# Optimization experiments

Hardware: AMD Instinct MI355X
Metric: run time of the kernel (lower is better)

The kernel has to match this reference:

```python
import itertools
import jax, jax.numpy as jnp
import numpy as np

# ---- constant tables / bases ----
Y_TABLE_NP = np.array([
    [16, 11, 10, 16, 24, 40, 51, 61],
    [12, 12, 14, 19, 26, 58, 60, 55],
    [14, 13, 16, 24, 40, 57, 69, 56],
    [14, 17, 22, 29, 51, 87, 80, 62],
    [18, 22, 37, 56, 68, 109, 103, 77],
    [24, 35, 55, 64, 81, 104, 113, 92],
    [49, 64, 78, 87, 103, 121, 120, 101],
    [72, 92, 95, 98, 112, 100, 103, 99]], dtype=np.float32)
C_TABLE_NP = np.full((8, 8), 99, dtype=np.float32)
C_TABLE_NP[:4, :4] = np.array([[17, 18, 24, 47], [18, 21, 26, 66],
                               [24, 26, 56, 99], [47, 66, 99, 99]], dtype=np.float32)

def _bases():
    dct = np.zeros((8, 8, 8, 8), dtype=np.float32)
    idct = np.zeros((8, 8, 8, 8), dtype=np.float32)
    for x, y, u, v in itertools.product(range(8), repeat=4):
        dct[x, y, u, v] = np.cos((2 * x + 1) * u * np.pi / 16) * np.cos((2 * y + 1) * v * np.pi / 16)
        idct[x, y, u, v] = np.cos((2 * u + 1) * x * np.pi / 16) * np.cos((2 * v + 1) * y * np.pi / 16)
    alpha = np.array([1.0 / np.sqrt(2)] + [1.0] * 7, dtype=np.float32)
    ao = np.outer(alpha, alpha).astype(np.float32)
    return jnp.asarray(dct), jnp.asarray(ao * 0.25), jnp.asarray(idct), jnp.asarray(ao)

DCT_T, DCT_SCALE, IDCT_T, ALPHA = _bases()
FACTOR = 0.4  # quality_to_factor(80) = (200 - 2*80)/100


def diff_round(x):
    r = jnp.round(x)
    return r + (x - r) ** 3


def _blocks(img):  # (B,H,W) -> (B, H*W/64, 8, 8)
    B, H, W = img.shape
    return img.reshape(B, H // 8, 8, W // 8, 8).transpose(0, 1, 3, 2, 4).reshape(B, -1, 8, 8)


def _merge(patches, H, W):  # (B, N, 8, 8) -> (B, H, W)
    B = patches.shape[0]
    return patches.reshape(B, H // 8, W // 8, 8, 8).transpose(0, 1, 3, 2, 4).reshape(B, H, W)


def setup_inputs() -> dict:
    key = jax.random.key(0)
    image = jax.random.uniform(key, (32, 3, 512, 512), dtype=jnp.float32)
    return {"image": image,
            "y_table": jnp.asarray(Y_TABLE_NP),
            "c_table": jnp.asarray(C_TABLE_NP)}


def reference(image, y_table, c_table):
    B, _, H, W = image.shape
    x = image * 255.0
    # RGB -> YCbCr (matrix stored transposed in torch, tensordot over channel)
    rgb2ycc = jnp.array([[0.299, 0.587, 0.114],
                         [-0.168736, -0.331264, 0.5],
                         [0.5, -0.418688, -0.081312]], dtype=jnp.float32)
    shift = jnp.array([0.0, 128.0, 128.0], dtype=jnp.float32)
    ycc = jnp.einsum('bchw,kc->bhwk', x, rgb2ycc) + shift  # (B,H,W,3)
    y = ycc[..., 0]
    # chroma subsampling: 2x2 average pool
    def pool2(ch):
        return ch.reshape(B, H // 2, 2, W // 2, 2).mean(axis=(2, 4))
    cb = pool2(ycc[..., 1])
    cr = pool2(ycc[..., 2])

    def compress(ch, table):
        blk = _blocks(ch) - 128.0
        d = DCT_SCALE * jnp.einsum('bnxy,xyuv->bnuv', blk, DCT_T)
        return diff_round(d / (table * FACTOR))

    yq = compress(y, y_table)
    cbq = compress(cb, c_table)
    crq = compress(cr, c_table)

    def decompress(q, table, h, w):
        d = (q * (table * FACTOR)) * ALPHA
        blk = 0.25 * jnp.einsum('bnuv,uvxy->bnxy', d, IDCT_T) + 128.0
        return _merge(blk, h, w)

    y_rec = decompress(yq, y_table, H, W)
    cb_rec = decompress(cbq, c_table, H // 2, W // 2)
    cr_rec = decompress(crq, c_table, H // 2, W // 2)

    def up2(ch):
        b, h, w = ch.shape
        return jnp.broadcast_to(ch[:, :, None, :, None], (b, h, 2, w, 2)).reshape(b, 2 * h, 2 * w)

    ycc_rec = jnp.stack([y_rec, up2(cb_rec), up2(cr_rec)], axis=-1)  # (B,H,W,3)
    ycc2rgb = jnp.array([[1.0, 0.0, 1.402],
                         [1.0, -0.344136, -0.714136],
                         [1.0, 1.772, 0.0]], dtype=jnp.float32)
    shift2 = jnp.array([0.0, -128.0, -128.0], dtype=jnp.float32)
    rgb = jnp.einsum('bhwk,ck->bhwc', ycc_rec + shift2, ycc2rgb)
    rgb = rgb.transpose(0, 3, 1, 2)  # (B,3,H,W)
    return jnp.clip(rgb, 0.0, 255.0) / 255.0
```

## Files before the change

kernel.cpp:

```cpp
#include <hip/hip_runtime.h>
#include <math.h>

#define IMG_H 512
#define IMG_W 512
#define IMG_HW (IMG_H * IMG_W)

namespace {

constexpr float CFv[9] = {
    1.0f,
    0.98078528040323044913f,
    0.92387953251128675613f,
    0.83146961230254523708f,
    0.70710678118654752440f,
    0.55557023301960222474f,
    0.38268343236508977173f,
    0.19509032201612826785f,
    0.0f
};

struct CTab {
    float  cf[8][8];
    double cd[8][8];
    float  aof[8][8];
    float  scalef[8][8];
};

constexpr CTab make_ctab() {
    CTab t{};
    for (int y = 0; y < 8; y++) {
        for (int v = 0; v < 8; v++) {
            int a = ((2 * y + 1) * v) & 31;
            if (a > 16) a = 32 - a;
            float val = (a <= 8) ? CFv[a] : -CFv[16 - a];
            t.cf[y][v] = val;
            t.cd[y][v] = (double)val;
        }
    }
    constexpr float A0 = 0.70710678118654752440f;
    for (int u = 0; u < 8; u++) {
        for (int v = 0; v < 8; v++) {
            float au = (u == 0) ? A0 : 1.0f;
            float av = (v == 0) ? A0 : 1.0f;
            float ao = au * av;
            t.aof[u][v] = ao;
            t.scalef[u][v] = ao * 0.25f;
        }
    }
    return t;
}

constexpr CTab CT = make_ctab();

constexpr double YC0 = (double)0.299f    * 255.0;
constexpr double YC1 = (double)0.587f    * 255.0;
constexpr double YC2 = (double)0.114f    * 255.0;
constexpr double CB0 = (double)-0.168736f * 255.0;
constexpr double CB1 = (double)-0.331264f * 255.0;
constexpr double CB2 = (double)0.5f      * 255.0;
constexpr double CR0 = (double)0.5f      * 255.0;
constexpr double CR1 = (double)-0.418688f * 255.0;
constexpr double CR2 = (double)-0.081312f * 255.0;

#define OFF_CBP 8448
#define OFF_CRP 10624
#define OFF_QY  12800
#define OFF_QC  13952
#define SMEM_BYTES 15104

__device__ __forceinline__ void xpose8_d(double v[8]) {
    const int l = threadIdx.x & 7;
    #pragma unroll
    for (int m = 1; m < 8; m <<= 1) {
        #pragma unroll
        for (int k = 0; k < 8; k++) {
            if ((k & m) == 0) {
                const int kp = k | m;
                double send = (l & m) ? v[k] : v[kp];
                double recv = __shfl_xor(send, m);
                v[k]  = (l & m) ? recv : v[k];
                v[kp] = (l & m) ? v[kp] : recv;
            }
        }
    }
}

__device__ __forceinline__ void xpose8_f(float v[8]) {
    const int l = threadIdx.x & 7;
    #pragma unroll
    for (int m = 1; m < 8; m <<= 1) {
        #pragma unroll
        for (int k = 0; k < 8; k++) {
            if ((k & m) == 0) {
                const int kp = k | m;
                float send = (l & m) ? v[k] : v[kp];
                float recv = __shfl_xor(send, m);
                v[k]  = (l & m) ? recv : v[k];
                v[kp] = (l & m) ? v[kp] : recv;
            }
        }
    }
}

}

__global__ void __launch_bounds__(256, 6) djpeg_kernel(
    const float* __restrict__ img,
    const float* __restrict__ ytab,
    const float* __restrict__ ctab,
    float* __restrict__ out)
{
    __shared__ __align__(16) unsigned char smem[SMEM_BYTES];
    double* lY  = (double*)(smem);
    double* cbP = (double*)(smem + OFF_CBP);
    double* crP = (double*)(smem + OFF_CRP);
    double* qY  = (double*)(smem + OFF_QY);
    double* qC  = (double*)(smem + OFF_QC);
    float* yR  = (float*)(smem);
    float* cbR = (float*)(smem + 4224);
    float* crR = (float*)(smem + 5312);

    const int t  = threadIdx.x;
    const int X0 = blockIdx.x * 64;
    const int Y0 = blockIdx.y * 16;
    const int bi = blockIdx.z;

    if (t < 128) {
        const float* tab = (t < 64) ? ytab : ctab;
        double* q = (t < 64) ? qY : qC;
        int e = t & 63, u = e >> 3, v = e & 7;
        float tfacf = tab[e] * 0.4f;
        double tf = (double)tfacf;
        q[v * 18 + 2 * u]     = (double)CT.scalef[u][v] / tf;
        q[v * 18 + 2 * u + 1] = tf * (double)CT.aof[u][v];
    }

    {
        const int x = t & 63, yb = t >> 6;
        double accb[2] = {0.0, 0.0}, accr[2] = {0.0, 0.0};
        size_t base = ((size_t)bi * 3) * IMG_HW + (size_t)Y0 * IMG_W + X0 + x;
        #pragma unroll
        for (int i = 0; i < 4; i++) {
            int y = yb * 4 + i;
            size_t p = base + (size_t)y * IMG_W;
            double R = (double)img[p];
            double G = (double)img[p + IMG_HW];
            double B = (double)img[p + 2 * IMG_HW];
            double Yv = YC0 * R + YC1 * G + YC2 * B - 128.0;
            double Cb = CB0 * R + CB1 * G + CB2 * B;
            double Cr = CR0 * R + CR1 * G + CR2 * B;
            lY[y * 66 + x] = Yv;
            accb[i >> 1] += Cb;
            accr[i >> 1] += Cr;
        }
        #pragma unroll
        for (int p2 = 0; p2 < 2; p2++) {
            double hb = accb[p2] + __shfl_xor(accb[p2], 1);
            double hr = accr[p2] + __shfl_xor(accr[p2], 1);
            if ((x & 1) == 0) {
                int pr = yb * 2 + p2;
                cbP[pr * 34 + (x >> 1)] = hb * 0.25;
                crP[pr * 34 + (x >> 1)] = hr * 0.25;
            }
        }
    }
    __syncthreads();

    const bool act = (t < 192);
    const int r = t & 7;
    const double* src = lY;
    const double* qtab = qY;
    float* dstR = yR;
    if (act) {
        if (t < 128) {
            int g = t >> 3, by = g >> 3, bx = g & 7;
            src  = lY + (by * 8 + r) * 66 + bx * 8;
            dstR = yR + (by * 8 + r) * 66 + bx * 8;
            qtab = qY;
        } else {
            int c = t - 128;
            int isCr = c >> 5;
            int g2 = (c >> 3) & 3;
            src  = (isCr ? crP : cbP) + r * 34 + g2 * 8;
            dstR = (isCr ? crR : cbR) + r * 34 + g2 * 8;
            qtab = qC;
        }
    }
    const float addv = (t < 128) ? 128.0f : 0.0f;

    double s1[8];
    if (act) {
        double a[8];
        #pragma unroll
        for (int y = 0; y < 8; y++) a[y] = src[y];
        double e[4], o[4];
        #pragma unroll
        for (int i = 0; i < 4; i++) { e[i] = a[i] + a[7 - i]; o[i] = a[i] - a[7 - i]; }
        #pragma unroll
        for (int v = 0; v < 8; v += 2) {
            s1[v]     = e[0] * CT.cd[0][v]     + e[1] * CT.cd[1][v]     + e[2] * CT.cd[2][v]     + e[3] * CT.cd[3][v];
            s1[v + 1] = o[0] * CT.cd[0][v + 1] + o[1] * CT.cd[1][v + 1] + o[2] * CT.cd[2][v + 1] + o[3] * CT.cd[3][v + 1];
        }
        xpose8_d(s1);
    }

    float mrow[8];
    if (act) {
        double e[4], o[4];
        #pragma unroll
        for (int i = 0; i < 4; i++) { e[i] = s1[i] + s1[7 - i]; o[i] = s1[i] - s1[7 - i]; }
        double D[8];
        #pragma unroll
        for (int u = 0; u < 8; u += 2) {
            D[u]     = e[0] * CT.cd[0][u]     + e[1] * CT.cd[1][u]     + e[2] * CT.cd[2][u]     + e[3] * CT.cd[3][u];
            D[u + 1] = o[0] * CT.cd[0][u + 1] + o[1] * CT.cd[1][u + 1] + o[2] * CT.cd[2][u + 1] + o[3] * CT.cd[3][u + 1];
        }
        float dq[8];
        #pragma unroll
        for (int u = 0; u < 8; u++) {
            double fs = qtab[r * 18 + 2 * u];
            double ds = qtab[r * 18 + 2 * u + 1];
            double xq = D[u] * fs;
            double rq = rint(xq);
            double ee = xq - rq;
            dq[u] = (float)((rq + ee * ee * ee) * ds);
        }
        #pragma unroll
        for (int x = 0; x < 4; x++) {
            float E = dq[0] * CT.cf[x][0] + dq[2] * CT.cf[x][2] + dq[4] * CT.cf[x][4] + dq[6] * CT.cf[x][6];
            float O = dq[1] * CT.cf[x][1] + dq[3] * CT.cf[x][3] + dq[5] * CT.cf[x][5] + dq[7] * CT.cf[x][7];
            mrow[x]     = E + O;
            mrow[7 - x] = E - O;
        }
        xpose8_f(mrow);
    }

    __syncthreads();

    if (act) {
        #pragma unroll
        for (int y = 0; y < 4; y++) {
            float E = mrow[0] * CT.cf[y][0] + mrow[2] * CT.cf[y][2] + mrow[4] * CT.cf[y][4] + mrow[6] * CT.cf[y][6];
            float O = mrow[1] * CT.cf[y][1] + mrow[3] * CT.cf[y][3] + mrow[5] * CT.cf[y][5] + mrow[7] * CT.cf[y][7];
            dstR[y]     = 0.25f * (E + O) + addv;
            dstR[7 - y] = 0.25f * (E - O) + addv;
        }
    }
    __syncthreads();

    {
        const int x = t & 63, yb = t >> 6;
        size_t base = ((size_t)bi * 3) * IMG_HW + (size_t)Y0 * IMG_W + X0 + x;
        #pragma unroll
        for (int i = 0; i < 4; i++) {
            int y = yb * 4 + i;
            float Yv = yR[y * 66 + x];
            float Cb = cbR[(y >> 1) * 34 + (x >> 1)];
            float Cr = crR[(y >> 1) * 34 + (x >> 1)];
            float Rr = fmaf(1.402f, Cr, Yv);
            float Gg = Yv - 0.344136f * Cb - 0.714136f * Cr;
            float Bb = fmaf(1.772f, Cb, Yv);
            Rr = fminf(fmaxf(Rr, 0.0f), 255.0f) * (1.0f / 255.0f);
            Gg = fminf(fmaxf(Gg, 0.0f), 255.0f) * (1.0f / 255.0f);
            Bb = fminf(fmaxf(Bb, 0.0f), 255.0f) * (1.0f / 255.0f);
            size_t p = base + (size_t)y * IMG_W;
            out[p] = Rr;
            out[p + IMG_HW] = Gg;
            out[p + 2 * IMG_HW] = Bb;
        }
    }
}

extern "C" void kernel_launch(void* const* d_in, const int* in_sizes, int n_in,
                              void* d_out, int out_size, void* d_ws, size_t ws_size,
                              hipStream_t stream) {
    (void)n_in; (void)out_size; (void)d_ws; (void)ws_size;
    const float* img = (const float*)d_in[0];
    const float* yt  = (const float*)d_in[1];
    const float* ct  = (const float*)d_in[2];
    float* out = (float*)d_out;
    int B = in_sizes[0] / (3 * IMG_HW);
    dim3 grid(IMG_W / 64, IMG_H / 16, B);
    djpeg_kernel<<<grid, dim3(256, 1, 1), 0, stream>>>(img, yt, ct, out);
}
```

Before: 185.1 us.

## Widen tile to 128 columns, process two DCT blocks per thread, vectorize I/O

Each block now covers a 16x128 tile instead of 16x64, halving the grid. Every active thread transforms two 8x8 blocks (luma plus a second luma or chroma block), so all 192 active threads do twice the work. Global loads and stores use float4, and the chroma 2x2 averaging now uses a shuffle across half-waves. Shared memory nearly doubles and launch bounds drop to 4 blocks per SM, which reduces occupancy while raising per-thread ILP and memory transaction width.

```diff
diff --git a/kernel.cpp b/kernel.cpp
--- a/kernel.cpp
+++ b/kernel.cpp
@@ -52,21 +52,23 @@
 
 constexpr CTab CT = make_ctab();
 
-constexpr double YC0 = (double)0.299f    * 255.0;
-constexpr double YC1 = (double)0.587f    * 255.0;
-constexpr double YC2 = (double)0.114f    * 255.0;
+constexpr double YC0 = (double)0.299f     * 255.0;
+constexpr double YC1 = (double)0.587f     * 255.0;
+constexpr double YC2 = (double)0.114f     * 255.0;
 constexpr double CB0 = (double)-0.168736f * 255.0;
 constexpr double CB1 = (double)-0.331264f * 255.0;
-constexpr double CB2 = (double)0.5f      * 255.0;
-constexpr double CR0 = (double)0.5f      * 255.0;
+constexpr double CB2 = (double)0.5f       * 255.0;
+constexpr double CR0 = (double)0.5f       * 255.0;
 constexpr double CR1 = (double)-0.418688f * 255.0;
 constexpr double CR2 = (double)-0.081312f * 255.0;
 
-#define OFF_CBP 8448
-#define OFF_CRP 10624
-#define OFF_QY  12800
-#define OFF_QC  13952
-#define SMEM_BYTES 15104
+#define OFF_CBP 16640
+#define OFF_CRP 20864
+#define OFF_QY  25088
+#define OFF_QC  26240
+#define SMEM_BYTES 27392
+#define OFF_CBR 8448
+#define OFF_CRR 10560
 
 __device__ __forceinline__ void xpose8_d(double v[8]) {
     const int l = threadIdx.x & 7;
@@ -102,9 +104,58 @@
     }
 }
 
-}
-
-__global__ void __launch_bounds__(256, 6) djpeg_kernel(
+__device__ __forceinline__ void fdct8_d(const double a[8], double s[8]) {
+    double e[4], o[4];
+    #pragma unroll
+    for (int i = 0; i < 4; i++) { e[i] = a[i] + a[7 - i]; o[i] = a[i] - a[7 - i]; }
+    #pragma unroll
+    for (int v = 0; v < 8; v += 2) {
+        s[v]     = e[0] * CT.cd[0][v]     + e[1] * CT.cd[1][v]     + e[2] * CT.cd[2][v]     + e[3] * CT.cd[3][v];
+        s[v + 1] = o[0] * CT.cd[0][v + 1] + o[1] * CT.cd[1][v + 1] + o[2] * CT.cd[2][v + 1] + o[3] * CT.cd[3][v + 1];
+    }
+}
+
+__device__ __forceinline__ void quant_idct_u(const double s1[8], const double* qtab, int r, float m[8]) {
+    double e[4], o[4];
+    #pragma unroll
+    for (int i = 0; i < 4; i++) { e[i] = s1[i] + s1[7 - i]; o[i] = s1[i] - s1[7 - i]; }
+    double D[8];
+    #pragma unroll
+    for (int u = 0; u < 8; u += 2) {
+        D[u]     = e[0] * CT.cd[0][u]     + e[1] * CT.cd[1][u]     + e[2] * CT.cd[2][u]     + e[3] * CT.cd[3][u];
+        D[u + 1] = o[0] * CT.cd[0][u + 1] + o[1] * CT.cd[1][u + 1] + o[2] * CT.cd[2][u + 1] + o[3] * CT.cd[3][u + 1];
+    }
+    float dq[8];
+    #pragma unroll
+    for (int u = 0; u < 8; u++) {
+        double2 q = *(const double2*)&qtab[r * 18 + 2 * u];
+        double xq = D[u] * q.x;
+        double rq = rint(xq);
+        double ee = xq - rq;
+        dq[u] = (float)((rq + ee * ee * ee) * q.y);
+    }
+    #pragma unroll
+    for (int x = 0; x < 4; x++) {
+        float E = dq[0] * CT.cf[x][0] + dq[2] * CT.cf[x][2] + dq[4] * CT.cf[x][4] + dq[6] * CT.cf[x][6];
+        float O = dq[1] * CT.cf[x][1] + dq[3] * CT.cf[x][3] + dq[5] * CT.cf[x][5] + dq[7] * CT.cf[x][7];
+        m[x]     = E + O;
+        m[7 - x] = E - O;
+    }
+}
+
+__device__ __forceinline__ void idct_v_store(const float m[8], float* dst, float addv) {
+    #pragma unroll
+    for (int y = 0; y < 4; y++) {
+        float E = m[0] * CT.cf[y][0] + m[2] * CT.cf[y][2] + m[4] * CT.cf[y][4] + m[6] * CT.cf[y][6];
+        float O = m[1] * CT.cf[y][1] + m[3] * CT.cf[y][3] + m[5] * CT.cf[y][5] + m[7] * CT.cf[y][7];
+        dst[y]     = 0.25f * (E + O) + addv;
+        dst[7 - y] = 0.25f * (E - O) + addv;
+    }
+}
+
+}
+
+__global__ void __launch_bounds__(256, 4) djpeg_kernel(
     const float* __restrict__ img,
     const float* __restrict__ ytab,
     const float* __restrict__ ctab,
@@ -117,11 +168,11 @@
     double* qY  = (double*)(smem + OFF_QY);
     double* qC  = (double*)(smem + OFF_QC);
     float* yR  = (float*)(smem);
-    float* cbR = (float*)(smem + 4224);
-    float* crR = (float*)(smem + 5312);
+    float* cbR = (float*)(smem + OFF_CBR);
+    float* crR = (float*)(smem + OFF_CRR);
 
     const int t  = threadIdx.x;
-    const int X0 = blockIdx.x * 64;
+    const int X0 = blockIdx.x * 128;
     const int Y0 = blockIdx.y * 16;
     const int bi = blockIdx.z;
 
@@ -136,31 +187,39 @@
     }
 
     {
-        const int x = t & 63, yb = t >> 6;
-        double accb[2] = {0.0, 0.0}, accr[2] = {0.0, 0.0};
-        size_t base = ((size_t)bi * 3) * IMG_HW + (size_t)Y0 * IMG_W + X0 + x;
-        #pragma unroll
-        for (int i = 0; i < 4; i++) {
-            int y = yb * 4 + i;
+        const int xg = t & 31, row0 = t >> 5;
+        size_t base = ((size_t)bi * 3) * IMG_HW + (size_t)Y0 * IMG_W + X0 + 4 * xg;
+        #pragma unroll
+        for (int i = 0; i < 2; i++) {
+            int y = row0 + 8 * i;
             size_t p = base + (size_t)y * IMG_W;
-            double R = (double)img[p];
-            double G = (double)img[p + IMG_HW];
-            double B = (double)img[p + 2 * IMG_HW];
-            double Yv = YC0 * R + YC1 * G + YC2 * B - 128.0;
-            double Cb = CB0 * R + CB1 * G + CB2 * B;
-            double Cr = CR0 * R + CR1 * G + CR2 * B;
-            lY[y * 66 + x] = Yv;
-            accb[i >> 1] += Cb;
-            accr[i >> 1] += Cr;
-        }
-        #pragma unroll
-        for (int p2 = 0; p2 < 2; p2++) {
-            double hb = accb[p2] + __shfl_xor(accb[p2], 1);
-            double hr = accr[p2] + __shfl_xor(accr[p2], 1);
-            if ((x & 1) == 0) {
-                int pr = yb * 2 + p2;
-                cbP[pr * 34 + (x >> 1)] = hb * 0.25;
-                crP[pr * 34 + (x >> 1)] = hr * 0.25;
+            const float4 Rv = *(const float4*)(img + p);
+            const float4 Gv = *(const float4*)(img + p + IMG_HW);
+            const float4 Bv = *(const float4*)(img + p + 2 * IMG_HW);
+            const float rr[4] = {Rv.x, Rv.y, Rv.z, Rv.w};
+            const float gg[4] = {Gv.x, Gv.y, Gv.z, Gv.w};
+            const float bb[4] = {Bv.x, Bv.y, Bv.z, Bv.w};
+            double Yd[4], Cbv[4], Crv[4];
+            #pragma unroll
+            for (int k = 0; k < 4; k++) {
+                double R = (double)rr[k], G = (double)gg[k], B = (double)bb[k];
+                Yd[k]  = YC0 * R + YC1 * G + YC2 * B - 128.0;
+                Cbv[k] = CB0 * R + CB1 * G + CB2 * B;
+                Crv[k] = CR0 * R + CR1 * G + CR2 * B;
+            }
+            double2* w = (double2*)&lY[y * 130 + 4 * xg];
+            w[0] = make_double2(Yd[0], Yd[1]);
+            w[1] = make_double2(Yd[2], Yd[3]);
+            double cb01 = Cbv[0] + Cbv[1], cb23 = Cbv[2] + Cbv[3];
+            double cr01 = Crv[0] + Crv[1], cr23 = Crv[2] + Crv[3];
+            cb01 += __shfl_xor(cb01, 32);
+            cb23 += __shfl_xor(cb23, 32);
+            cr01 += __shfl_xor(cr01, 32);
+            cr23 += __shfl_xor(cr23, 32);
+            if ((t & 32) == 0) {
+                int yh = y >> 1;
+                *(double2*)&cbP[yh * 66 + 2 * xg] = make_double2(cb01 * 0.25, cb23 * 0.25);
+                *(double2*)&crP[yh * 66 + 2 * xg] = make_double2(cr01 * 0.25, cr23 * 0.25);
             }
         }
     }
@@ -168,105 +227,89 @@
 
     const bool act = (t < 192);
     const int r = t & 7;
-    const double* src = lY;
-    const double* qtab = qY;
-    float* dstR = yR;
+    const int g0 = t >> 3;
+    const double* src0 = lY;  const double* src1 = lY;
+    const double* qt1 = qY;
+    float* dst0 = yR;  float* dst1 = yR;
+    float addv1 = 128.0f;
     if (act) {
-        if (t < 128) {
-            int g = t >> 3, by = g >> 3, bx = g & 7;
-            src  = lY + (by * 8 + r) * 66 + bx * 8;
-            dstR = yR + (by * 8 + r) * 66 + bx * 8;
-            qtab = qY;
+        {
+            int by = (g0 >> 4), bx = g0 & 15;
+            src0 = lY + (by * 8 + r) * 130 + bx * 8;
+            dst0 = yR + (by * 8 + r) * 132 + bx * 8;
+        }
+        int g1 = g0 + 24;
+        if (g1 < 32) {
+            int bx = g1 - 16;
+            src1 = lY + (8 + r) * 130 + bx * 8;
+            dst1 = yR + (8 + r) * 132 + bx * 8;
+            qt1 = qY; addv1 = 128.0f;
+        } else if (g1 < 40) {
+            int bx = g1 - 32;
+            src1 = cbP + r * 66 + bx * 8;
+            dst1 = cbR + r * 66 + bx * 8;
+            qt1 = qC; addv1 = 0.0f;
         } else {
-            int c = t - 128;
-            int isCr = c >> 5;
-            int g2 = (c >> 3) & 3;
-            src  = (isCr ? crP : cbP) + r * 34 + g2 * 8;
-            dstR = (isCr ? crR : cbR) + r * 34 + g2 * 8;
-            qtab = qC;
-        }
-    }
-    const float addv = (t < 128) ? 128.0f : 0.0f;
-
-    double s1[8];
+            int bx = g1 - 40;
+            src1 = crP + r * 66 + bx * 8;
+            dst1 = crR + r * 66 + bx * 8;
+            qt1 = qC; addv1 = 0.0f;
+        }
+    }
+
+    double s1a[8], s1b[8];
     if (act) {
-        double a[8];
-        #pragma unroll
-        for (int y = 0; y < 8; y++) a[y] = src[y];
-        double e[4], o[4];
-        #pragma unroll
-        for (int i = 0; i < 4; i++) { e[i] = a[i] + a[7 - i]; o[i] = a[i] - a[7 - i]; }
-        #pragma unroll
-        for (int v = 0; v < 8; v += 2) {
-            s1[v]     = e[0] * CT.cd[0][v]     + e[1] * CT.cd[1][v]     + e[2] * CT.cd[2][v]     + e[3] * CT.cd[3][v];
-            s1[v + 1] = o[0] * CT.cd[0][v + 1] + o[1] * CT.cd[1][v + 1] + o[2] * CT.cd[2][v + 1] + o[3] * CT.cd[3][v + 1];
-        }
-        xpose8_d(s1);
-    }
-
-    float mrow[8];
+        double a[8], b[8];
+        #pragma unroll
+        for (int y = 0; y < 8; y++) { a[y] = src0[y]; b[y] = src1[y]; }
+        fdct8_d(a, s1a);
+        fdct8_d(b, s1b);
+        xpose8_d(s1a);
+        xpose8_d(s1b);
+    }
+    float ma[8], mb[8];
     if (act) {
-        double e[4], o[4];
-        #pragma unroll
-        for (int i = 0; i < 4; i++) { e[i] = s1[i] + s1[7 - i]; o[i] = s1[i] - s1[7 - i]; }
-        double D[8];
-        #pragma unroll
-        for (int u = 0; u < 8; u += 2) {
-            D[u]     = e[0] * CT.cd[0][u]     + e[1] * CT.cd[1][u]     + e[2] * CT.cd[2][u]     + e[3] * CT.cd[3][u];
-            D[u + 1] = o[0] * CT.cd[0][u + 1] + o[1] * CT.cd[1][u + 1] + o[2] * CT.cd[2][u + 1] + o[3] * CT.cd[3][u + 1];
-        }
-        float dq[8];
-        #pragma unroll
-        for (int u = 0; u < 8; u++) {
-            double fs = qtab[r * 18 + 2 * u];
-            double ds = qtab[r * 18 + 2 * u + 1];
-            double xq = D[u] * fs;
-            double rq = rint(xq);
-            double ee = xq - rq;
-            dq[u] = (float)((rq + ee * ee * ee) * ds);
-        }
-        #pragma unroll
-        for (int x = 0; x < 4; x++) {
-            float E = dq[0] * CT.cf[x][0] + dq[2] * CT.cf[x][2] + dq[4] * CT.cf[x][4] + dq[6] * CT.cf[x][6];
-            float O = dq[1] * CT.cf[x][1] + dq[3] * CT.cf[x][3] + dq[5] * CT.cf[x][5] + dq[7] * CT.cf[x][7];
-            mrow[x]     = E + O;
-            mrow[7 - x] = E - O;
-        }
-        xpose8_f(mrow);
-    }
-
+        quant_idct_u(s1a, qY, r, ma);
+        quant_idct_u(s1b, qt1, r, mb);
+        xpose8_f(ma);
+        xpose8_f(mb);
+    }
     __syncthreads();
 
     if (act) {
-        #pragma unroll
-        for (int y = 0; y < 4; y++) {
-            float E = mrow[0] * CT.cf[y][0] + mrow[2] * CT.cf[y][2] + mrow[4] * CT.cf[y][4] + mrow[6] * CT.cf[y][6];
-            float O = mrow[1] * CT.cf[y][1] + mrow[3] * CT.cf[y][3] + mrow[5] * CT.cf[y][5] + mrow[7] * CT.cf[y][7];
-            dstR[y]     = 0.25f * (E + O) + addv;
-            dstR[7 - y] = 0.25f * (E - O) + addv;
-        }
+        idct_v_store(ma, dst0, 128.0f);
+        idct_v_store(mb, dst1, addv1);
     }
     __syncthreads();
 
     {
-        const int x = t & 63, yb = t >> 6;
-        size_t base = ((size_t)bi * 3) * IMG_HW + (size_t)Y0 * IMG_W + X0 + x;
-        #pragma unroll
-        for (int i = 0; i < 4; i++) {
-            int y = yb * 4 + i;
-            float Yv = yR[y * 66 + x];
-            float Cb = cbR[(y >> 1) * 34 + (x >> 1)];
-            float Cr = crR[(y >> 1) * 34 + (x >> 1)];
-            float Rr = fmaf(1.402f, Cr, Yv);
-            float Gg = Yv - 0.344136f * Cb - 0.714136f * Cr;
-            float Bb = fmaf(1.772f, Cb, Yv);
-            Rr = fminf(fmaxf(Rr, 0.0f), 255.0f) * (1.0f / 255.0f);
-            Gg = fminf(fmaxf(Gg, 0.0f), 255.0f) * (1.0f / 255.0f);
-            Bb = fminf(fmaxf(Bb, 0.0f), 255.0f) * (1.0f / 255.0f);
+        const int xg = t & 31, row0 = t >> 5;
+        size_t base = ((size_t)bi * 3) * IMG_HW + (size_t)Y0 * IMG_W + X0 + 4 * xg;
+        #pragma unroll
+        for (int i = 0; i < 2; i++) {
+            int y = row0 + 8 * i;
+            float4 yv = *(const float4*)&yR[y * 132 + 4 * xg];
+            int yh = y >> 1;
+            float2 cbv = *(const float2*)&cbR[yh * 66 + 2 * xg];
+            float2 crv = *(const float2*)&crR[yh * 66 + 2 * xg];
+            const float ya[4] = {yv.x, yv.y, yv.z, yv.w};
+            float ro[4], go[4], bo[4];
+            #pragma unroll
+            for (int k = 0; k < 4; k++) {
+                float Cb = (k < 2) ? cbv.x : cbv.y;
+                float Cr = (k < 2) ? crv.x : crv.y;
+                float Yv = ya[k];
+                float Rr = fmaf(1.402f, Cr, Yv);
+                float Gg = Yv - 0.344136f * Cb - 0.714136f * Cr;
+                float Bb = fmaf(1.772f, Cb, Yv);
+                ro[k] = fminf(fmaxf(Rr, 0.0f), 255.0f) * (1.0f / 255.0f);
+                go[k] = fminf(fmaxf(Gg, 0.0f), 255.0f) * (1.0f / 255.0f);
+                bo[k] = fminf(fmaxf(Bb, 0.0f), 255.0f) * (1.0f / 255.0f);
+            }
             size_t p = base + (size_t)y * IMG_W;
-            out[p] = Rr;
-            out[p + IMG_HW] = Gg;
-            out[p + 2 * IMG_HW] = Bb;
+            *(float4*)(out + p)              = make_float4(ro[0], ro[1], ro[2], ro[3]);
+            *(float4*)(out + p + IMG_HW)     = make_float4(go[0], go[1], go[2], go[3]);
+            *(float4*)(out + p + 2 * IMG_HW) = make_float4(bo[0], bo[1], bo[2], bo[3]);
         }
     }
 }
@@ -280,6 +323,6 @@
     const float* ct  = (const float*)d_in[2];
     float* out = (float*)d_out;
     int B = in_sizes[0] / (3 * IMG_HW);
-    dim3 grid(IMG_W / 64, IMG_H / 16, B);
+    dim3 grid(IMG_W / 128, IMG_H / 16, B);
     djpeg_kernel<<<grid, dim3(256, 1, 1), 0, stream>>>(img, yt, ct, out);
 }
```

Result: slower. 211.3 us (+14.1%).
